# Kernel optimization log

Hardware: AMD Instinct MI355X
Metric: run time of the kernel (lower is better)

The kernel has to match this reference:

```python
import jax, jax.numpy as jnp
from jax import lax
import numpy as np

# Mask type 'A' for 7x7 conv: rows above center, left of center in center row; center excluded.
_m = np.zeros((7, 7), np.float32)
_m[:3, :] = 1.0
_m[3, :3] = 1.0
MASK_A = jnp.asarray(_m)


def masked_conv7(x, w, b):
    # x: [B,1,H,W], w: [16,1,7,7]
    wm = w * MASK_A[None, None]
    y = lax.conv_general_dilated(x, wm, (1, 1), [(3, 3), (3, 3)],
                                 dimension_numbers=("NCHW", "OIHW", "NCHW"))
    return y + b[None, :, None, None]


def skew(x):
    # [B,C,H,W] -> [B,C,H,H+W-1], row i shifted right by i (diagonals -> columns)
    B, C, H, W = x.shape
    rows = jnp.arange(H)[:, None]
    cols = rows + jnp.arange(W)[None, :]
    out = jnp.zeros((B, C, H, H + W - 1), x.dtype)
    return out.at[:, :, rows, cols].set(x)


def unskew(xs, W):
    B, C, H, _ = xs.shape
    rows = jnp.arange(H)[:, None]
    cols = rows + jnp.arange(W)[None, :]
    return xs[:, :, rows, cols]


def diag_lstm(x, wi, bi, ws0, ws1):
    # One direction of the diagonal LSTM. x: [B,16,H,W]
    B, C, H, W = x.shape
    xs = skew(x)  # [B,16,H,T], T = H+W-1
    # 1x1 input-to-state conv over the whole skewed map (precomputed)
    i2s = jnp.einsum("oc,bcht->boht", wi, xs) + bi[None, :, None, None]  # [B,64,H,T]

    def step(carry, col):
        h, c = carry  # [B,16,H] each
        # 2x1 state-to-state conv along height (causal downward): taps h[i], h[i-1]
        h_up = jnp.pad(h, ((0, 0), (0, 0), (1, 0)))[:, :, :-1]
        s = col + jnp.einsum("oc,bch->boh", ws1, h) + jnp.einsum("oc,bch->boh", ws0, h_up)
        o, f, i, g = jnp.split(s, 4, axis=1)
        c = jax.nn.sigmoid(f) * c + jax.nn.sigmoid(i) * jnp.tanh(g)
        h = jax.nn.sigmoid(o) * jnp.tanh(c)
        return (h, c), h

    cols = jnp.moveaxis(i2s, 3, 0)  # [T,B,64,H]
    z = jnp.zeros((B, C, H), x.dtype)
    _, hs = lax.scan(step, (z, z), cols)  # [T,B,16,H]
    hs = jnp.moveaxis(hs, 0, 3)  # [B,16,H,T]
    return unskew(hs, W)


def bilstm_layer(x, wi2, bi2, w02, w12):
    fwd = diag_lstm(x, wi2[0], bi2[0], w02[0], w12[0])
    xr = x[:, :, :, ::-1]
    bwd = diag_lstm(xr, wi2[1], bi2[1], w02[1], w12[1])[:, :, :, ::-1]
    # shift right-to-left output down one row to preserve causality
    bwd = jnp.pad(bwd, ((0, 0), (0, 0), (1, 0), (0, 0)))[:, :, :-1, :]
    return x + fwd + bwd  # residual


def pixelrnn_fwd(X, conv_in_w, conv_in_b, rnn_i2s_w, rnn_i2s_b, rnn_ss_w0, rnn_ss_w1,
                 out_w1, out_b1, out_w2, out_b2, out_w3, out_b3):
    h = masked_conv7(X, conv_in_w, conv_in_b)
    for l in range(7):
        h = bilstm_layer(h, rnn_i2s_w[l], rnn_i2s_b[l], rnn_ss_w0[l], rnn_ss_w1[l])
    for w, b in ((out_w1, out_b1), (out_w2, out_b2)):
        h = jax.nn.relu(jnp.einsum("oc,bchw->bohw", w, h) + b[None, :, None, None])
    return jnp.einsum("oc,bchw->bohw", out_w3, h) + out_b3[None, :, None, None]


def setup_inputs() -> dict:
    key = jax.random.key(0)
    ks = jax.random.split(key, 10)
    B, H, W = 32, 64, 64
    s = 0.25  # ~1/sqrt(16) init scale
    return {
        "X": jax.random.normal(ks[0], (B, 1, H, W), jnp.float32),
        "conv_in_w": jax.random.normal(ks[1], (16, 1, 7, 7), jnp.float32) * 0.15,
        "conv_in_b": jnp.zeros((16,), jnp.float32),
        "rnn_i2s_w": jax.random.normal(ks[2], (7, 2, 64, 16), jnp.float32) * s,
        "rnn_i2s_b": jnp.zeros((7, 2, 64), jnp.float32),
        "rnn_ss_w0": jax.random.normal(ks[3], (7, 2, 64, 16), jnp.float32) * s,
        "rnn_ss_w1": jax.random.normal(ks[4], (7, 2, 64, 16), jnp.float32) * s,
        "out_w1": jax.random.normal(ks[5], (16, 16), jnp.float32) * s,
        "out_b1": jnp.zeros((16,), jnp.float32),
        "out_w2": jax.random.normal(ks[6], (16, 16), jnp.float32) * s,
        "out_b2": jnp.zeros((16,), jnp.float32),
        "out_w3": jax.random.normal(ks[7], (1, 16), jnp.float32) * s,
        "out_b3": jnp.zeros((1,), jnp.float32),
    }


def reference(X, conv_in_w, conv_in_b, rnn_i2s_w, rnn_i2s_b, rnn_ss_w0, rnn_ss_w1,
              out_w1, out_b1, out_w2, out_b2, out_w3, out_b3):
    return pixelrnn_fwd(X, conv_in_w, conv_in_b, rnn_i2s_w, rnn_i2s_b, rnn_ss_w0,
                        rnn_ss_w1, out_w1, out_b1, out_w2, out_b2, out_w3, out_b3)
```

## Files before the change

kernel.cpp:

```cpp
#include <hip/hip_runtime.h>

#define DI __device__ __forceinline__

typedef __bf16 bf16x8 __attribute__((ext_vector_type(8)));
typedef float f32x4 __attribute__((ext_vector_type(4)));
typedef unsigned short u16x8 __attribute__((ext_vector_type(8)));
typedef unsigned short u16x4 __attribute__((ext_vector_type(4)));

DI float frcp(float x) { return __builtin_amdgcn_rcpf(x); }
DI float fsig(float x) { return frcp(1.0f + __expf(-x)); }
DI float ftanh(float x) { return 1.0f - 2.0f * frcp(1.0f + __expf(2.0f * x)); }

__global__ __launch_bounds__(256) void k_conv(const float* __restrict__ X,
                                              const float* __restrict__ Wc,
                                              const float* __restrict__ Bc,
                                              float* __restrict__ xo) {
    int n = blockIdx.x * 256 + threadIdx.x;
    int xx = n & 63, yy = (n >> 6) & 63, b = n >> 12;
    float acc[16];
#pragma unroll
    for (int o = 0; o < 16; ++o) acc[o] = Bc[o];
    const float* Xb = X + (size_t)b * 4096;
#pragma unroll
    for (int ky = 0; ky < 4; ++ky) {
        int yi = yy + ky - 3;
        if (yi < 0) continue;
        int kxmax = (ky == 3) ? 3 : 7;
        for (int kx = 0; kx < kxmax; ++kx) {
            int xi = xx + kx - 3;
            if (xi < 0 || xi > 63) continue;
            float v = Xb[yi * 64 + xi];
#pragma unroll
            for (int o = 0; o < 16; ++o)
                acc[o] = fmaf(Wc[o * 49 + ky * 7 + kx], v, acc[o]);
        }
    }
    float4* xp = reinterpret_cast<float4*>(xo + (size_t)n * 16);
#pragma unroll
    for (int q = 0; q < 4; ++q) {
        float4 t; t.x = acc[q*4]; t.y = acc[q*4+1]; t.z = acc[q*4+2]; t.w = acc[q*4+3];
        xp[q] = t;
    }
}

__global__ __launch_bounds__(256) void k_prep(float* __restrict__ x,
                                              const float* __restrict__ fwd,
                                              const float* __restrict__ bwdr,
                                              const float* __restrict__ wi_all,
                                              int layer, int addflag,
                                              float* __restrict__ G) {
    __shared__ float wsh[2048];
    for (int i = threadIdx.x; i < 2048; i += 256)
        wsh[i] = wi_all[layer * 2048 + i];
    __syncthreads();

    int n = blockIdx.x * 256 + threadIdx.x;
    int w = n & 63, r = (n >> 6) & 63, b = n >> 12;
    size_t pix = (size_t)n;

    float v[16];
    const float4* xp = reinterpret_cast<const float4*>(x + pix * 16);
#pragma unroll
    for (int q = 0; q < 4; ++q) {
        float4 t = xp[q];
        v[q*4] = t.x; v[q*4+1] = t.y; v[q*4+2] = t.z; v[q*4+3] = t.w;
    }
    if (addflag) {
        const float4* fp = reinterpret_cast<const float4*>(fwd + pix * 16);
#pragma unroll
        for (int q = 0; q < 4; ++q) {
            float4 t = fp[q];
            v[q*4] += t.x; v[q*4+1] += t.y; v[q*4+2] += t.z; v[q*4+3] += t.w;
        }
        if (r > 0) {
            const float4* bp = reinterpret_cast<const float4*>(bwdr + (pix - 64) * 16);
#pragma unroll
            for (int q = 0; q < 4; ++q) {
                float4 t = bp[q];
                v[q*4] += t.x; v[q*4+1] += t.y; v[q*4+2] += t.z; v[q*4+3] += t.w;
            }
        }
        float4* xps = reinterpret_cast<float4*>(x + pix * 16);
#pragma unroll
        for (int q = 0; q < 4; ++q) {
            float4 t; t.x = v[q*4]; t.y = v[q*4+1]; t.z = v[q*4+2]; t.w = v[q*4+3];
            xps[q] = t;
        }
    }

#pragma unroll
    for (int dir = 0; dir < 2; ++dir) {
        const float* wp = wsh + dir * 1024;
        int wg = dir ? (63 - w) : w;
#pragma unroll
        for (int c0g = 0; c0g < 4; ++c0g) {
            float val[16];
#pragma unroll
            for (int mb = 0; mb < 4; ++mb) {
#pragma unroll
                for (int reg = 0; reg < 4; ++reg) {
                    int g = mb * 16 + c0g * 4 + reg;
                    const float4* wr = reinterpret_cast<const float4*>(wp + g * 16);
                    float s = 0.f;
#pragma unroll
                    for (int c4 = 0; c4 < 4; ++c4) {
                        float4 a = wr[c4];
                        s = fmaf(a.x, v[c4*4+0], s);
                        s = fmaf(a.y, v[c4*4+1], s);
                        s = fmaf(a.z, v[c4*4+2], s);
                        s = fmaf(a.w, v[c4*4+3], s);
                    }
                    val[mb * 4 + reg] = s;
                }
            }
            float4* dst = reinterpret_cast<float4*>(
                G + ((((size_t)(dir * 32 + b) * 64 + r) * 4 + c0g) * 64 + wg) * 16);
#pragma unroll
            for (int q = 0; q < 4; ++q) {
                float4 t; t.x = val[q*4]; t.y = val[q*4+1]; t.z = val[q*4+2]; t.w = val[q*4+3];
                dst[q] = t;
            }
        }
    }
}

__global__ __launch_bounds__(256) void k_scan(const float* __restrict__ G,
                                              const float* __restrict__ w0_all,
                                              const float* __restrict__ w1_all,
                                              const float* __restrict__ bi_all,
                                              int layer,
                                              float* __restrict__ fwdbuf,
                                              float* __restrict__ bwdbuf) {
    int dir = blockIdx.x >> 5, b = blockIdx.x & 31;
    int t = threadIdx.x;
    int wv = t >> 6;
    int l = t & 63;
    int kb = l >> 4;
    int m = l & 15;
    int r = wv * 16 + m;
    int wb_ = (layer * 2 + dir) * 1024;

    const float* Wsel = (kb < 2 ? w1_all : w0_all) + wb_;
    int koff = (kb & 1) * 8;
    bf16x8 ahi[4], alo[4];
#pragma unroll
    for (int mb = 0; mb < 4; ++mb) {
        const float* wr = Wsel + (mb * 16 + m) * 16 + koff;
#pragma unroll
        for (int j = 0; j < 8; ++j) {
            float wv_ = wr[j];
            __bf16 hi = (__bf16)wv_;
            ahi[mb][j] = hi;
            alo[mb][j] = (__bf16)(wv_ - (float)hi);
        }
    }
    f32x4 biasv[4];
#pragma unroll
    for (int mb = 0; mb < 4; ++mb)
#pragma unroll
        for (int j = 0; j < 4; ++j)
            biasv[mb][j] = bi_all[(layer * 2 + dir) * 64 + mb * 16 + kb * 4 + j];

    __shared__ __align__(16) unsigned short hbuf[2][2][65 * 24];
    for (int i = t; i < 2 * 2 * 65 * 24; i += 256) (&hbuf[0][0][0])[i] = 0;

    const float* Glane = G + (((size_t)(dir * 32 + b) * 64 + r) * 4 + kb) * 1024;
    float* ob = dir ? bwdbuf : fwdbuf;
    const size_t obase = (size_t)b * 65536;

    float cst[4] = {0.f, 0.f, 0.f, 0.f};
    f32x4 gr[4];
#pragma unroll
    for (int q = 0; q < 4; ++q) gr[q] = (f32x4){0.f, 0.f, 0.f, 0.f};
    if (r == 0) {
        const f32x4* gp = reinterpret_cast<const f32x4*>(Glane);
#pragma unroll
        for (int q = 0; q < 4; ++q) gr[q] = gp[q];
    }
    __syncthreads();

    int p = 0;
#pragma unroll 1
    for (int tt = 0; tt < 127; ++tt) {
        f32x4 nr[4];
#pragma unroll
        for (int q = 0; q < 4; ++q) nr[q] = (f32x4){0.f, 0.f, 0.f, 0.f};
        int wn = tt + 1 - r;
        if ((unsigned)wn < 64u) {
            const f32x4* gp = reinterpret_cast<const f32x4*>(Glane + (size_t)wn * 16);
#pragma unroll
            for (int q = 0; q < 4; ++q) nr[q] = gp[q];
        }

        int q = r + 1 - (kb >> 1);
        int boff = q * 24 + (kb & 1) * 8;
        u16x8 bh_raw = *reinterpret_cast<const u16x8*>(&hbuf[p][0][boff]);
        u16x8 bl_raw = *reinterpret_cast<const u16x8*>(&hbuf[p][1][boff]);
        bf16x8 bhi = __builtin_bit_cast(bf16x8, bh_raw);
        bf16x8 blo = __builtin_bit_cast(bf16x8, bl_raw);

        f32x4 acc[4];
#pragma unroll
        for (int mb = 0; mb < 4; ++mb) acc[mb] = biasv[mb] + gr[mb];
#pragma unroll
        for (int mb = 0; mb < 4; ++mb)
            acc[mb] = __builtin_amdgcn_mfma_f32_16x16x32_bf16(ahi[mb], bhi, acc[mb], 0, 0, 0);
#pragma unroll
        for (int mb = 0; mb < 4; ++mb)
            acc[mb] = __builtin_amdgcn_mfma_f32_16x16x32_bf16(ahi[mb], blo, acc[mb], 0, 0, 0);
#pragma unroll
        for (int mb = 0; mb < 4; ++mb)
            acc[mb] = __builtin_amdgcn_mfma_f32_16x16x32_bf16(alo[mb], bhi, acc[mb], 0, 0, 0);

        int wcur = tt - r;
        bool vout = (unsigned)wcur < 64u;
        float hv[4];
        u16x4 hih, lol;
#pragma unroll
        for (int j = 0; j < 4; ++j) {
            float so = acc[0][j], sf = acc[1][j], si = acc[2][j], sg = acc[3][j];
            float cn = fsig(sf) * cst[j] + fsig(si) * ftanh(sg);
            cst[j] = cn;
            float hn = fsig(so) * ftanh(cn);
            hv[j] = hn;
            __bf16 hi = (__bf16)hn;
            hih[j] = __builtin_bit_cast(unsigned short, hi);
            lol[j] = __builtin_bit_cast(unsigned short, (__bf16)(hn - (float)hi));
        }
        int widx = (r + 1) * 24 + kb * 4;
        *reinterpret_cast<u16x4*>(&hbuf[p ^ 1][0][widx]) = hih;
        *reinterpret_cast<u16x4*>(&hbuf[p ^ 1][1][widx]) = lol;
        if (vout) {
            int wo = dir ? (63 - wcur) : wcur;
            float4 hq; hq.x = hv[0]; hq.y = hv[1]; hq.z = hv[2]; hq.w = hv[3];
            *reinterpret_cast<float4*>(ob + obase + ((size_t)((r << 6) + wo) << 4) + kb * 4) = hq;
        }
#pragma unroll
        for (int qq = 0; qq < 4; ++qq) gr[qq] = nr[qq];

        asm volatile("s_waitcnt lgkmcnt(0)" ::: "memory");
        __builtin_amdgcn_sched_barrier(0);
        __builtin_amdgcn_s_barrier();
        __builtin_amdgcn_sched_barrier(0);
        p ^= 1;
    }
}

__global__ __launch_bounds__(256) void k_head(const float* __restrict__ x,
                                              const float* __restrict__ fwd,
                                              const float* __restrict__ bwdr,
                                              const float* __restrict__ W1,
                                              const float* __restrict__ B1,
                                              const float* __restrict__ W2,
                                              const float* __restrict__ B2,
                                              const float* __restrict__ W3,
                                              const float* __restrict__ B3,
                                              float* __restrict__ out) {
    int n = blockIdx.x * 256 + threadIdx.x;
    int r = (n >> 6) & 63;
    size_t pix = (size_t)n;
    float v[16];
    const float4* xp = reinterpret_cast<const float4*>(x + pix * 16);
#pragma unroll
    for (int q = 0; q < 4; ++q) {
        float4 t = xp[q];
        v[q*4] = t.x; v[q*4+1] = t.y; v[q*4+2] = t.z; v[q*4+3] = t.w;
    }
    const float4* fp = reinterpret_cast<const float4*>(fwd + pix * 16);
#pragma unroll
    for (int q = 0; q < 4; ++q) {
        float4 t = fp[q];
        v[q*4] += t.x; v[q*4+1] += t.y; v[q*4+2] += t.z; v[q*4+3] += t.w;
    }
    if (r > 0) {
        const float4* bp = reinterpret_cast<const float4*>(bwdr + (pix - 64) * 16);
#pragma unroll
        for (int q = 0; q < 4; ++q) {
            float4 t = bp[q];
            v[q*4] += t.x; v[q*4+1] += t.y; v[q*4+2] += t.z; v[q*4+3] += t.w;
        }
    }
    float h1[16];
#pragma unroll
    for (int o = 0; o < 16; ++o) {
        float a = B1[o];
#pragma unroll
        for (int c = 0; c < 16; ++c) a = fmaf(W1[o * 16 + c], v[c], a);
        h1[o] = fmaxf(a, 0.f);
    }
    float h2[16];
#pragma unroll
    for (int o = 0; o < 16; ++o) {
        float a = B2[o];
#pragma unroll
        for (int c = 0; c < 16; ++c) a = fmaf(W2[o * 16 + c], h1[c], a);
        h2[o] = fmaxf(a, 0.f);
    }
    float y = B3[0];
#pragma unroll
    for (int c = 0; c < 16; ++c) y = fmaf(W3[c], h2[c], y);
    out[pix] = y;
}

extern "C" void kernel_launch(void* const* d_in, const int* in_sizes, int n_in,
                              void* d_out, int out_size, void* d_ws, size_t ws_size,
                              hipStream_t stream) {
    const float* X  = (const float*)d_in[0];
    const float* cw = (const float*)d_in[1];
    const float* cb = (const float*)d_in[2];
    const float* wi = (const float*)d_in[3];
    const float* bi = (const float*)d_in[4];
    const float* w0 = (const float*)d_in[5];
    const float* w1 = (const float*)d_in[6];
    const float* W1 = (const float*)d_in[7];
    const float* B1 = (const float*)d_in[8];
    const float* W2 = (const float*)d_in[9];
    const float* B2 = (const float*)d_in[10];
    const float* W3 = (const float*)d_in[11];
    const float* B3 = (const float*)d_in[12];
    float* out = (float*)d_out;

    char* ws = (char*)d_ws;
    float* x   = (float*)ws;
    float* fwd = (float*)(ws + ((size_t)8 << 20));
    float* bwd = (float*)(ws + ((size_t)16 << 20));
    float* G   = (float*)(ws + ((size_t)24 << 20));

    k_conv<<<512, 256, 0, stream>>>(X, cw, cb, x);
    for (int l = 0; l < 7; ++l) {
        k_prep<<<512, 256, 0, stream>>>(x, fwd, bwd, wi, l, l > 0 ? 1 : 0, G);
        k_scan<<<64, 256, 0, stream>>>(G, w0, w1, bi, l, fwd, bwd);
    }
    k_head<<<512, 256, 0, stream>>>(x, fwd, bwd, W1, B1, W2, B2, W3, B3, out);
}
```

Baseline: 1.201 ms.

## Fuse input-to-state projection and residual add into the scan kernel via MFMA

Removes the separate k_prep kernel that materialized the 64-channel input-to-state tensor G in global memory. The scan kernel now loads the 16-channel residual input plus the previous forward/backward outputs per diagonal step, sums them, and computes the i2s projection with extra bf16 MFMAs using a hi/lo split. Ping-pong buffers for V, fwd and bwd avoid read/write races between layers. This cuts global traffic and a launch per layer, but adds MFMAs and loads onto the serial critical path of the scan, which runs on only 64 blocks.

```diff
diff --git a/kernel.cpp b/kernel.cpp
--- a/kernel.cpp
+++ b/kernel.cpp
@@ -43,94 +43,17 @@
     }
 }
 
-__global__ __launch_bounds__(256) void k_prep(float* __restrict__ x,
-                                              const float* __restrict__ fwd,
-                                              const float* __restrict__ bwdr,
-                                              const float* __restrict__ wi_all,
-                                              int layer, int addflag,
-                                              float* __restrict__ G) {
-    __shared__ float wsh[2048];
-    for (int i = threadIdx.x; i < 2048; i += 256)
-        wsh[i] = wi_all[layer * 2048 + i];
-    __syncthreads();
-
-    int n = blockIdx.x * 256 + threadIdx.x;
-    int w = n & 63, r = (n >> 6) & 63, b = n >> 12;
-    size_t pix = (size_t)n;
-
-    float v[16];
-    const float4* xp = reinterpret_cast<const float4*>(x + pix * 16);
-#pragma unroll
-    for (int q = 0; q < 4; ++q) {
-        float4 t = xp[q];
-        v[q*4] = t.x; v[q*4+1] = t.y; v[q*4+2] = t.z; v[q*4+3] = t.w;
-    }
-    if (addflag) {
-        const float4* fp = reinterpret_cast<const float4*>(fwd + pix * 16);
-#pragma unroll
-        for (int q = 0; q < 4; ++q) {
-            float4 t = fp[q];
-            v[q*4] += t.x; v[q*4+1] += t.y; v[q*4+2] += t.z; v[q*4+3] += t.w;
-        }
-        if (r > 0) {
-            const float4* bp = reinterpret_cast<const float4*>(bwdr + (pix - 64) * 16);
-#pragma unroll
-            for (int q = 0; q < 4; ++q) {
-                float4 t = bp[q];
-                v[q*4] += t.x; v[q*4+1] += t.y; v[q*4+2] += t.z; v[q*4+3] += t.w;
-            }
-        }
-        float4* xps = reinterpret_cast<float4*>(x + pix * 16);
-#pragma unroll
-        for (int q = 0; q < 4; ++q) {
-            float4 t; t.x = v[q*4]; t.y = v[q*4+1]; t.z = v[q*4+2]; t.w = v[q*4+3];
-            xps[q] = t;
-        }
-    }
-
-#pragma unroll
-    for (int dir = 0; dir < 2; ++dir) {
-        const float* wp = wsh + dir * 1024;
-        int wg = dir ? (63 - w) : w;
-#pragma unroll
-        for (int c0g = 0; c0g < 4; ++c0g) {
-            float val[16];
-#pragma unroll
-            for (int mb = 0; mb < 4; ++mb) {
-#pragma unroll
-                for (int reg = 0; reg < 4; ++reg) {
-                    int g = mb * 16 + c0g * 4 + reg;
-                    const float4* wr = reinterpret_cast<const float4*>(wp + g * 16);
-                    float s = 0.f;
-#pragma unroll
-                    for (int c4 = 0; c4 < 4; ++c4) {
-                        float4 a = wr[c4];
-                        s = fmaf(a.x, v[c4*4+0], s);
-                        s = fmaf(a.y, v[c4*4+1], s);
-                        s = fmaf(a.z, v[c4*4+2], s);
-                        s = fmaf(a.w, v[c4*4+3], s);
-                    }
-                    val[mb * 4 + reg] = s;
-                }
-            }
-            float4* dst = reinterpret_cast<float4*>(
-                G + ((((size_t)(dir * 32 + b) * 64 + r) * 4 + c0g) * 64 + wg) * 16);
-#pragma unroll
-            for (int q = 0; q < 4; ++q) {
-                float4 t; t.x = val[q*4]; t.y = val[q*4+1]; t.z = val[q*4+2]; t.w = val[q*4+3];
-                dst[q] = t;
-            }
-        }
-    }
-}
-
-__global__ __launch_bounds__(256) void k_scan(const float* __restrict__ G,
-                                              const float* __restrict__ w0_all,
-                                              const float* __restrict__ w1_all,
-                                              const float* __restrict__ bi_all,
-                                              int layer,
-                                              float* __restrict__ fwdbuf,
-                                              float* __restrict__ bwdbuf) {
+__global__ __launch_bounds__(256, 1) void k_scan(const float* __restrict__ Vin,
+                                                 float* __restrict__ Vout,
+                                                 const float* __restrict__ fwdIn,
+                                                 const float* __restrict__ bwdIn,
+                                                 float* __restrict__ fwdOut,
+                                                 float* __restrict__ bwdOut,
+                                                 const float* __restrict__ wi_all,
+                                                 const float* __restrict__ w0_all,
+                                                 const float* __restrict__ w1_all,
+                                                 const float* __restrict__ bi_all,
+                                                 int layer, int first) {
     int dir = blockIdx.x >> 5, b = blockIdx.x & 31;
     int t = threadIdx.x;
     int wv = t >> 6;
@@ -154,6 +77,22 @@
             alo[mb][j] = (__bf16)(wv_ - (float)hi);
         }
     }
+
+    const float* Wi = wi_all + wb_;
+    int cbase = (kb & 1) * 8;
+    bf16x8 wihi[4], wiloz[4];
+#pragma unroll
+    for (int mb = 0; mb < 4; ++mb) {
+        const float* wr = Wi + (mb * 16 + m) * 16 + cbase;
+#pragma unroll
+        for (int j = 0; j < 8; ++j) {
+            float wv_ = wr[j];
+            __bf16 hi = (__bf16)wv_;
+            wihi[mb][j] = hi;
+            wiloz[mb][j] = (kb < 2) ? (__bf16)(wv_ - (float)hi) : (__bf16)0.f;
+        }
+    }
+
     f32x4 biasv[4];
 #pragma unroll
     for (int mb = 0; mb < 4; ++mb)
@@ -164,33 +103,90 @@
     __shared__ __align__(16) unsigned short hbuf[2][2][65 * 24];
     for (int i = t; i < 2 * 2 * 65 * 24; i += 256) (&hbuf[0][0][0])[i] = 0;
 
-    const float* Glane = G + (((size_t)(dir * 32 + b) * 64 + r) * 4 + kb) * 1024;
-    float* ob = dir ? bwdbuf : fwdbuf;
-    const size_t obase = (size_t)b * 65536;
+    const size_t rowbase  = ((size_t)b * 64 + r) * 64;
+    const size_t rowbaseU = ((size_t)b * 64 + (r - 1)) * 64;
+    float* ob = dir ? bwdOut : fwdOut;
+    bool vstore_lane = (!first) && (dir == 0) && (kb < 2);
+    bool fb_load = !first;
+    bool b_load = fb_load && (r > 0);
 
     float cst[4] = {0.f, 0.f, 0.f, 0.f};
-    f32x4 gr[4];
-#pragma unroll
-    for (int q = 0; q < 4; ++q) gr[q] = (f32x4){0.f, 0.f, 0.f, 0.f};
-    if (r == 0) {
-        const f32x4* gp = reinterpret_cast<const f32x4*>(Glane);
-#pragma unroll
-        for (int q = 0; q < 4; ++q) gr[q] = gp[q];
+
+    f32x4 xc[2], fc[2], bc[2];
+    {
+        int w = 0 - r;
+        bool valid = (unsigned)w < 64u;
+#pragma unroll
+        for (int q = 0; q < 2; ++q) { xc[q] = (f32x4){0,0,0,0}; fc[q] = (f32x4){0,0,0,0}; bc[q] = (f32x4){0,0,0,0}; }
+        if (valid) {
+            int wimg = dir ? (63 - w) : w;
+            const f32x4* px = reinterpret_cast<const f32x4*>(Vin + (rowbase + wimg) * 16 + cbase);
+            xc[0] = px[0]; xc[1] = px[1];
+            if (fb_load) {
+                const f32x4* pf = reinterpret_cast<const f32x4*>(fwdIn + (rowbase + wimg) * 16 + cbase);
+                fc[0] = pf[0]; fc[1] = pf[1];
+                if (b_load) {
+                    const f32x4* pb = reinterpret_cast<const f32x4*>(bwdIn + (rowbaseU + wimg) * 16 + cbase);
+                    bc[0] = pb[0]; bc[1] = pb[1];
+                }
+            }
+        }
     }
     __syncthreads();
 
     int p = 0;
 #pragma unroll 1
     for (int tt = 0; tt < 127; ++tt) {
-        f32x4 nr[4];
-#pragma unroll
-        for (int q = 0; q < 4; ++q) nr[q] = (f32x4){0.f, 0.f, 0.f, 0.f};
-        int wn = tt + 1 - r;
-        if ((unsigned)wn < 64u) {
-            const f32x4* gp = reinterpret_cast<const f32x4*>(Glane + (size_t)wn * 16);
-#pragma unroll
-            for (int q = 0; q < 4; ++q) nr[q] = gp[q];
-        }
+        f32x4 xn[2], fn[2], bn[2];
+#pragma unroll
+        for (int q = 0; q < 2; ++q) { xn[q] = (f32x4){0,0,0,0}; fn[q] = (f32x4){0,0,0,0}; bn[q] = (f32x4){0,0,0,0}; }
+        {
+            int w = tt + 1 - r;
+            if ((unsigned)w < 64u) {
+                int wimg = dir ? (63 - w) : w;
+                const f32x4* px = reinterpret_cast<const f32x4*>(Vin + (rowbase + wimg) * 16 + cbase);
+                xn[0] = px[0]; xn[1] = px[1];
+                if (fb_load) {
+                    const f32x4* pf = reinterpret_cast<const f32x4*>(fwdIn + (rowbase + wimg) * 16 + cbase);
+                    fn[0] = pf[0]; fn[1] = pf[1];
+                    if (b_load) {
+                        const f32x4* pb = reinterpret_cast<const f32x4*>(bwdIn + (rowbaseU + wimg) * 16 + cbase);
+                        bn[0] = pb[0]; bn[1] = pb[1];
+                    }
+                }
+            }
+        }
+
+        int wcur = tt - r;
+        bool vout = (unsigned)wcur < 64u;
+        int wo = dir ? (63 - wcur) : wcur;
+
+        f32x4 v8[2];
+#pragma unroll
+        for (int q = 0; q < 2; ++q) v8[q] = xc[q] + fc[q] + bc[q];
+        bf16x8 vsel;
+#pragma unroll
+        for (int q = 0; q < 2; ++q)
+#pragma unroll
+            for (int j = 0; j < 4; ++j) {
+                float f = v8[q][j];
+                __bf16 hi = (__bf16)f;
+                vsel[q * 4 + j] = (kb < 2) ? hi : (__bf16)(f - (float)hi);
+            }
+        if (vstore_lane && vout) {
+            f32x4* pv = reinterpret_cast<f32x4*>(Vout + (rowbase + wo) * 16 + cbase);
+            pv[0] = v8[0]; pv[1] = v8[1];
+        }
+
+        f32x4 acc[4];
+#pragma unroll
+        for (int mb = 0; mb < 4; ++mb) acc[mb] = biasv[mb];
+#pragma unroll
+        for (int mb = 0; mb < 4; ++mb)
+            acc[mb] = __builtin_amdgcn_mfma_f32_16x16x32_bf16(wihi[mb], vsel, acc[mb], 0, 0, 0);
+#pragma unroll
+        for (int mb = 0; mb < 4; ++mb)
+            acc[mb] = __builtin_amdgcn_mfma_f32_16x16x32_bf16(wiloz[mb], vsel, acc[mb], 0, 0, 0);
 
         int q = r + 1 - (kb >> 1);
         int boff = q * 24 + (kb & 1) * 8;
@@ -198,10 +194,6 @@
         u16x8 bl_raw = *reinterpret_cast<const u16x8*>(&hbuf[p][1][boff]);
         bf16x8 bhi = __builtin_bit_cast(bf16x8, bh_raw);
         bf16x8 blo = __builtin_bit_cast(bf16x8, bl_raw);
-
-        f32x4 acc[4];
-#pragma unroll
-        for (int mb = 0; mb < 4; ++mb) acc[mb] = biasv[mb] + gr[mb];
 #pragma unroll
         for (int mb = 0; mb < 4; ++mb)
             acc[mb] = __builtin_amdgcn_mfma_f32_16x16x32_bf16(ahi[mb], bhi, acc[mb], 0, 0, 0);
@@ -212,8 +204,6 @@
         for (int mb = 0; mb < 4; ++mb)
             acc[mb] = __builtin_amdgcn_mfma_f32_16x16x32_bf16(alo[mb], bhi, acc[mb], 0, 0, 0);
 
-        int wcur = tt - r;
-        bool vout = (unsigned)wcur < 64u;
         float hv[4];
         u16x4 hih, lol;
 #pragma unroll
@@ -231,12 +221,11 @@
         *reinterpret_cast<u16x4*>(&hbuf[p ^ 1][0][widx]) = hih;
         *reinterpret_cast<u16x4*>(&hbuf[p ^ 1][1][widx]) = lol;
         if (vout) {
-            int wo = dir ? (63 - wcur) : wcur;
             float4 hq; hq.x = hv[0]; hq.y = hv[1]; hq.z = hv[2]; hq.w = hv[3];
-            *reinterpret_cast<float4*>(ob + obase + ((size_t)((r << 6) + wo) << 4) + kb * 4) = hq;
-        }
-#pragma unroll
-        for (int qq = 0; qq < 4; ++qq) gr[qq] = nr[qq];
+            *reinterpret_cast<float4*>(ob + (rowbase + wo) * 16 + kb * 4) = hq;
+        }
+#pragma unroll
+        for (int qq = 0; qq < 2; ++qq) { xc[qq] = xn[qq]; fc[qq] = fn[qq]; bc[qq] = bn[qq]; }
 
         asm volatile("s_waitcnt lgkmcnt(0)" ::: "memory");
         __builtin_amdgcn_sched_barrier(0);
@@ -321,15 +310,23 @@
     float* out = (float*)d_out;
 
     char* ws = (char*)d_ws;
-    float* x   = (float*)ws;
-    float* fwd = (float*)(ws + ((size_t)8 << 20));
-    float* bwd = (float*)(ws + ((size_t)16 << 20));
-    float* G   = (float*)(ws + ((size_t)24 << 20));
-
-    k_conv<<<512, 256, 0, stream>>>(X, cw, cb, x);
+    float* V0 = (float*)ws;
+    float* V1 = (float*)(ws + ((size_t)8 << 20));
+    float* f0 = (float*)(ws + ((size_t)16 << 20));
+    float* b0 = (float*)(ws + ((size_t)24 << 20));
+    float* f1 = (float*)(ws + ((size_t)32 << 20));
+    float* b1 = (float*)(ws + ((size_t)40 << 20));
+
+    k_conv<<<512, 256, 0, stream>>>(X, cw, cb, V0);
     for (int l = 0; l < 7; ++l) {
-        k_prep<<<512, 256, 0, stream>>>(x, fwd, bwd, wi, l, l > 0 ? 1 : 0, G);
-        k_scan<<<64, 256, 0, stream>>>(G, w0, w1, bi, l, fwd, bwd);
-    }
-    k_head<<<512, 256, 0, stream>>>(x, fwd, bwd, W1, B1, W2, B2, W3, B3, out);
+        const float* Vin = (l == 0) ? V0 : (((l - 1) & 1) ? V1 : V0);
+        float* Vout = (l == 0) ? V1 : ((l & 1) ? V1 : V0);
+        const float* fIn = ((l + 1) & 1) ? f1 : f0;
+        const float* bIn = ((l + 1) & 1) ? b1 : b0;
+        float* fOut = (l & 1) ? f1 : f0;
+        float* bOut = (l & 1) ? b1 : b0;
+        k_scan<<<64, 256, 0, stream>>>(Vin, Vout, fIn, bIn, fOut, bOut,
+                                       wi, w0, w1, bi, l, l == 0 ? 1 : 0);
+    }
+    k_head<<<512, 256, 0, stream>>>(V0, f0, b0, W1, B1, W2, B2, W3, B3, out);
 }
```

Measured after the change: 1.004 ms. 1.2x faster.
